# Kernel tuning notes

Hardware: AMD Instinct MI355X
Metric: run time of the kernel (lower is better)

## Reference

```python
import jax, jax.numpy as jnp
import numpy as np
from jax import lax

TOTAL_STEPS = 100
BETA_0 = 0.1
BETA_1 = 20.0


def setup_inputs() -> dict:
    key = jax.random.key(0)
    k1, k2 = jax.random.split(key)
    x = jax.random.normal(k1, (64, 256, 64), dtype=jnp.float32)
    noise = jax.random.normal(k2, (TOTAL_STEPS, 64, 256, 64), dtype=jnp.float32)
    return {"x": x, "noise": noise}


def reference(x, noise):
    # VP-SDE Euler-Maruyama forward diffusion, matching forward_sample.
    S = TOTAL_STEPS
    dt = jnp.float32(1.0 / S)
    sqrt_dt = jnp.sqrt(dt)
    # torch loop uses t in [1..S] and computes coefficients at (t-1)/S
    norm_t = (jnp.arange(S, dtype=jnp.float32)) / S  # (t-1)/S for t=1..S

    def step(x_prev, inp):
        nt, n = inp
        beta_t = BETA_0 + nt * (BETA_1 - BETA_0)
        drift = -0.5 * beta_t * x_prev
        x_t = x_prev + drift * dt + jnp.sqrt(beta_t) * n * sqrt_dt
        return x_t, x_t

    _, traj = lax.scan(step, x, (norm_t, noise))  # traj: (S, N, L, D)
    return jnp.concatenate([x[None], traj], axis=0)  # (S+1, N, L, D)
```

## Files before the change

kernel.cpp:

```cpp
#include <hip/hip_runtime.h>
#include <math.h>


#define S_STEPS 100
#define U 5
#define NW (S_STEPS / U)

typedef float f32x4 __attribute__((ext_vector_type(4)));

__global__ __launch_bounds__(256) void vpsde_fwd_kernel(
    const f32x4* __restrict__ x,
    const f32x4* __restrict__ noise,
    f32x4* __restrict__ out,
    int ne4)
{
    __shared__ float s_a[S_STEPS];
    __shared__ float s_b[S_STEPS];

    const int tid = threadIdx.x;
    if (tid < S_STEPS) {
        const float dt = 0.01f;
        float nt_ = (float)tid * dt;
        float beta = 0.1f + nt_ * 19.9f;
        s_a[tid] = 1.0f - 0.5f * beta * dt;
        s_b[tid] = sqrtf(beta) * 0.1f;
    }
    __syncthreads();

    const int idx = blockIdx.x * blockDim.x + tid;
    if (idx >= ne4) return;

    const f32x4* np_ = noise + idx;
    f32x4* op_ = out + idx;

    f32x4 xv = x[idx];
    __builtin_nontemporal_store(xv, op_);

    f32x4 A[U], B[U];

    auto loadw = [&](f32x4* buf, int w0) {
        #pragma unroll
        for (int k = 0; k < U; ++k)
            buf[k] = __builtin_nontemporal_load(np_ + (size_t)(w0 + k) * ne4);
    };
    auto consume = [&](const f32x4* buf, int w0) {
        #pragma unroll
        for (int k = 0; k < U; ++k) {
            const int t = w0 + k;
            const float a = s_a[t];
            const float b = s_b[t];
            xv = a * xv + b * buf[k];
            __builtin_nontemporal_store(xv, op_ + (size_t)(t + 1) * ne4);
        }
    };

    loadw(A, 0);
    for (int w = 0; w < NW; w += 2) {
        loadw(B, (w + 1) * U);
        consume(A, w * U);
        if (w + 2 < NW) loadw(A, (w + 2) * U);
        consume(B, (w + 1) * U);
    }
}

extern "C" void kernel_launch(void* const* d_in, const int* in_sizes, int n_in,
                              void* d_out, int out_size, void* d_ws, size_t ws_size,
                              hipStream_t stream) {
    const float* x     = (const float*)d_in[0];
    const float* noise = (const float*)d_in[1];
    float* out         = (float*)d_out;

    const int ne  = in_sizes[0];
    const int ne4 = ne / 4;

    const int block = 256;
    const int grid  = (ne4 + block - 1) / block;

    vpsde_fwd_kernel<<<grid, block, 0, stream>>>(
        (const f32x4*)x, (const f32x4*)noise, (f32x4*)out, ne4);
}
```

Baseline: 178.5 us.

## Stream noise through LDS via global_load_lds with manual vmcnt double buffering

Result: slower. 192.1 us (+7.6%).

```diff
diff --git a/kernel.cpp b/kernel.cpp
--- a/kernel.cpp
+++ b/kernel.cpp
@@ -1,66 +1,94 @@
 #include <hip/hip_runtime.h>
 #include <math.h>
+#include <stdint.h>
 
 
 #define S_STEPS 100
-#define U 5
-#define NW (S_STEPS / U)
+#define U 4
+#define NWIN (S_STEPS / U)
 
 typedef float f32x4 __attribute__((ext_vector_type(4)));
 
+#define WAITV(n) asm volatile("s_waitcnt vmcnt(" #n ")" ::: "memory")
+
+__device__ __forceinline__ void gl_lds16(const float* g, const float* l) {
+    __builtin_amdgcn_global_load_lds(
+        (const __attribute__((address_space(1))) unsigned int*)g,
+        (__attribute__((address_space(3))) unsigned int*)l,
+        16, 0, 0);
+}
+
 __global__ __launch_bounds__(256) void vpsde_fwd_kernel(
-    const f32x4* __restrict__ x,
-    const f32x4* __restrict__ noise,
-    f32x4* __restrict__ out,
-    int ne4)
+    const float* __restrict__ x,
+    const float* __restrict__ noise,
+    float* __restrict__ out,
+    int ne)
 {
-    __shared__ float s_a[S_STEPS];
-    __shared__ float s_b[S_STEPS];
+    __shared__ __align__(16) float s_noise[2][U][4][256];
+    __shared__ float2 s_ab[S_STEPS];
 
-    const int tid = threadIdx.x;
+    const int tid  = threadIdx.x;
+    const int wid  = tid >> 6;
+    const int lane = tid & 63;
+
     if (tid < S_STEPS) {
         const float dt = 0.01f;
-        float nt_ = (float)tid * dt;
+        float nt_  = (float)tid * dt;
         float beta = 0.1f + nt_ * 19.9f;
-        s_a[tid] = 1.0f - 0.5f * beta * dt;
-        s_b[tid] = sqrtf(beta) * 0.1f;
+        s_ab[tid] = make_float2(1.0f - 0.5f * beta * dt,
+                                sqrtf(beta) * 0.1f);
     }
     __syncthreads();
 
-    const int idx = blockIdx.x * blockDim.x + tid;
-    if (idx >= ne4) return;
+    const size_t idx4  = (size_t)blockIdx.x * 256 + tid;
+    const size_t plane = (size_t)ne;
 
-    const f32x4* np_ = noise + idx;
-    f32x4* op_ = out + idx;
+    f32x4 xv = *(const f32x4*)(x + idx4 * 4);
+    __builtin_nontemporal_store(xv, (f32x4*)(out + idx4 * 4));
 
-    f32x4 xv = x[idx];
-    __builtin_nontemporal_store(xv, op_);
+    const float* gld = noise + idx4 * 4;
+    float*       dst = out + plane + idx4 * 4;
 
-    f32x4 A[U], B[U];
-
-    auto loadw = [&](f32x4* buf, int w0) {
-        #pragma unroll
-        for (int k = 0; k < U; ++k)
-            buf[k] = __builtin_nontemporal_load(np_ + (size_t)(w0 + k) * ne4);
-    };
-    auto consume = [&](const f32x4* buf, int w0) {
+    auto issue = [&](int b) {
         #pragma unroll
         for (int k = 0; k < U; ++k) {
-            const int t = w0 + k;
-            const float a = s_a[t];
-            const float b = s_b[t];
-            xv = a * xv + b * buf[k];
-            __builtin_nontemporal_store(xv, op_ + (size_t)(t + 1) * ne4);
+            gl_lds16(gld, &s_noise[b][k][wid][0]);
+            gld += plane;
+        }
+    };
+    auto consume = [&](int b, int t0) {
+        #pragma unroll
+        for (int k = 0; k < U; ++k) {
+            float2 ab = s_ab[t0 + k];
+            f32x4 nv = *(const f32x4*)&s_noise[b][k][wid][lane * 4];
+            xv = ab.x * xv + ab.y * nv;
+            __builtin_nontemporal_store(xv, (f32x4*)dst);
+            dst += plane;
         }
     };
 
-    loadw(A, 0);
-    for (int w = 0; w < NW; w += 2) {
-        loadw(B, (w + 1) * U);
-        consume(A, w * U);
-        if (w + 2 < NW) loadw(A, (w + 2) * U);
-        consume(B, (w + 1) * U);
+    issue(0);
+    issue(1);
+
+    WAITV(4);
+    __builtin_amdgcn_sched_barrier(0);
+    consume(0, 0);
+    __builtin_amdgcn_sched_barrier(0);
+    issue(0);
+
+    int b = 1;
+    for (int w = 1; w <= NWIN - 2; ++w) {
+        WAITV(8);
+        __builtin_amdgcn_sched_barrier(0);
+        consume(b, w * U);
+        __builtin_amdgcn_sched_barrier(0);
+        if (w <= NWIN - 3) issue(b);
+        b ^= 1;
     }
+
+    WAITV(4);
+    __builtin_amdgcn_sched_barrier(0);
+    consume(b, (NWIN - 1) * U);
 }
 
 extern "C" void kernel_launch(void* const* d_in, const int* in_sizes, int n_in,
@@ -72,10 +100,8 @@
 
     const int ne  = in_sizes[0];
     const int ne4 = ne / 4;
+    const int block = 256;
+    const int grid  = ne4 / block;
 
-    const int block = 256;
-    const int grid  = (ne4 + block - 1) / block;
-
-    vpsde_fwd_kernel<<<grid, block, 0, stream>>>(
-        (const f32x4*)x, (const f32x4*)noise, (f32x4*)out, ne4);
+    vpsde_fwd_kernel<<<grid, block, 0, stream>>>(x, noise, out, ne);
 }
```
